# Performance work log

Measured on AMD Instinct MI355X. Metric: run time of the kernel, lower is better.

## Reference

```python
import jax, jax.numpy as jnp
import numpy as np
import math

B, S, DIM, H = 2, 2048, 1024, 16
DH = DIM // H          # 64, per-head dim
DFF = 2048             # FCLayer hidden
NEG = -1.0e9


def setup_inputs() -> dict:
    key = jax.random.key(0)
    ks = jax.random.split(key, 10)
    glorot = jax.nn.initializers.glorot_uniform()
    de_x = jax.random.normal(ks[0], (B, S, DIM), dtype=jnp.float32)
    en_x = jax.random.normal(ks[1], (B, S, DIM), dtype=jnp.float32)
    # causal mask: 1.0 where attention is disallowed (upper triangle)
    mask = jnp.triu(jnp.ones((S, S), dtype=jnp.float32), k=1)
    # Stacked per-head projection weights for the (shared) attn_heads.
    Wq = glorot(ks[2], (H, DIM, DH), jnp.float32)
    Wk = glorot(ks[3], (H, DIM, DH), jnp.float32)
    Wv = glorot(ks[4], (H, DIM, DH), jnp.float32)
    W1 = glorot(ks[5], (DIM, DFF), jnp.float32)
    b1 = jnp.zeros((DFF,), jnp.float32)
    W2 = glorot(ks[6], (DFF, DIM), jnp.float32)
    b2 = jnp.zeros((DIM,), jnp.float32)
    return {"de_x": de_x, "en_x": en_x, "mask": mask,
            "Wq": Wq, "Wk": Wk, "Wv": Wv,
            "W1": W1, "b1": b1, "W2": W2, "b2": b2}


def _multihead(q_x, k_x, v_x, Wq, Wk, Wv, mask):
    # q_x/k_x/v_x: [B,S,DIM]; W*: [H,DIM,DH]
    q = jnp.einsum('bsd,hde->bhse', q_x, Wq)
    k = jnp.einsum('bsd,hde->bhse', k_x, Wk)
    v = jnp.einsum('bsd,hde->bhse', v_x, Wv)
    p = jnp.einsum('bhse,bhte->bhst', q, k) / math.sqrt(DH)
    if mask is not None:
        p = p + mask * NEG
    p = jax.nn.softmax(p, axis=-1)
    h = jnp.einsum('bhst,bhte->bhse', p, v)      # [B,H,S,DH]
    # concat heads along feature dim -> [B,S,DIM]
    return h.transpose(0, 2, 1, 3).reshape(q_x.shape[0], q_x.shape[1], -1)


def reference(de_x, en_x, mask, Wq, Wk, Wv, W1, b1, W2, b2):
    # Faithful to the source: compute_multihead_output ignores its attn_heads
    # arg and always uses self.attn_heads, and binds head(q=outer_en, k=outer_en,
    # v=outer_de). So:
    #   h1 = MHA(q=de_x, k=de_x, v=de_x, mask) with attn_heads weights
    #   h2 = MHA(q=en_x, k=en_x, v=h1, None)   with the SAME weights
    h1 = _multihead(de_x, de_x, de_x, Wq, Wk, Wv, mask)
    h2 = _multihead(en_x, en_x, h1, Wq, Wk, Wv, None)
    ff1 = jax.nn.relu(h2 @ W1 + b1)
    y = ff1 @ W2 + b2
    return y
```

## Files before the change

### kernel.cpp

```cpp
#include <hip/hip_runtime.h>
#include <stdint.h>


#define DEV static __device__ __forceinline__

typedef __attribute__((ext_vector_type(8))) __bf16 bf16x8;
typedef __attribute__((ext_vector_type(8))) unsigned short u16x8;
typedef __attribute__((ext_vector_type(2))) uint32_t u32x2;
typedef __attribute__((ext_vector_type(4))) float f32x4;

DEV float bf2f(uint16_t u) { union { uint32_t u; float f; } v; v.u = ((uint32_t)u) << 16; return v.f; }
DEV uint16_t f2bf(float f) {
  union { float f; uint32_t u; } v; v.f = f;
  uint32_t r = v.u + 0x7fffu + ((v.u >> 16) & 1u);
  return (uint16_t)(r >> 16);
}
DEV uint16_t f2bf_hw(float f) { return __builtin_bit_cast(unsigned short, (__bf16)f); }

DEV bf16x8 asbf(u16x8 v) { return __builtin_bit_cast(bf16x8, v); }
DEV f32x4 mfma32(bf16x8 a, bf16x8 b, f32x4 c) {
  return __builtin_amdgcn_mfma_f32_16x16x32_bf16(a, b, c, 0, 0, 0);
}

DEV void gload_lds16(const void* g, void* l) {
  __builtin_amdgcn_global_load_lds(
      (const __attribute__((address_space(1))) uint32_t*)g,
      (__attribute__((address_space(3))) uint32_t*)l, 16, 0, 0);
}

DEV int swz(int row, int slot) { return slot ^ (row & 7); }

DEV bf16x8 frag8(const uint16_t* l, int row, int slot) {
  u16x8 v = *(const u16x8*)((const char*)l + row * 128 + (swz(row, slot) << 4));
  return asbf(v);
}

__global__ void probe_k(const uint32_t* __restrict__ mask, uint32_t* __restrict__ flag) {
  flag[0] = (mask[1] & 0xFFFFu) ? 1u : 0u;
}

__global__ __launch_bounds__(256) void cvt_k(const void* __restrict__ src,
                                             uint16_t* __restrict__ dst, int n,
                                             const uint32_t* __restrict__ flag) {
  const int isbf = (int)flag[0];
  const int stride = gridDim.x * 256 * 8;
  for (int i = (blockIdx.x * 256 + threadIdx.x) * 8; i < n; i += stride) {
    if (isbf) {
      *(u16x8*)(dst + i) = *(const u16x8*)((const uint16_t*)src + i);
    } else {
      const float* sf = (const float*)src + i;
      u16x8 o;
      for (int j = 0; j < 8; j++) o[j] = f2bf(sf[j]);
      *(u16x8*)(dst + i) = o;
    }
  }
}

__global__ __launch_bounds__(256) void transpose_k(const void* __restrict__ in_,
                                                   uint16_t* __restrict__ out, int R, int C,
                                                   float scale,
                                                   const uint32_t* __restrict__ flag) {
  __shared__ uint16_t t[32][33];
  const int isbf = (int)flag[0];
  const int b = blockIdx.z;
  const float* in_f = (const float*)in_ + (size_t)b * R * C;
  const uint16_t* in_u = (const uint16_t*)in_ + (size_t)b * R * C;
  out += (size_t)b * R * C;
  const int c0 = blockIdx.x * 32, r0 = blockIdx.y * 32;
  const int tx = threadIdx.x & 31, ty = threadIdx.x >> 5;
  for (int i = 0; i < 4; i++) {
    int r = ty + i * 8;
    size_t idx = (size_t)(r0 + r) * C + c0 + tx;
    uint16_t v;
    if (isbf) v = (scale == 1.0f) ? in_u[idx] : f2bf(bf2f(in_u[idx]) * scale);
    else      v = f2bf(in_f[idx] * scale);
    t[r][tx] = v;
  }
  __syncthreads();
  for (int i = 0; i < 4; i++) {
    int r = ty + i * 8;
    out[(size_t)(c0 + r) * R + r0 + tx] = t[tx][r];
  }
}

__global__ __launch_bounds__(256) void proj_k(
    const uint16_t* __restrict__ A_qk, const uint16_t* __restrict__ A_v,
    const uint16_t* __restrict__ Wt,
    uint16_t* __restrict__ Q, uint16_t* __restrict__ K, uint16_t* __restrict__ Vt) {
  __shared__ __attribute__((aligned(16))) uint16_t lA[2][128 * 64];
  __shared__ __attribute__((aligned(16))) uint16_t lB[2][128 * 64];
  const int tid = threadIdx.x, lane = tid & 63, wave = tid >> 6;
  const int g = lane >> 4;
  const int m0 = blockIdx.x * 128, n0 = blockIdx.y * 128;
  const int proj = n0 >> 10;
  const uint16_t* A = (proj == 2 ? A_v : A_qk);
  const uint16_t* Bt = Wt + (size_t)n0 * 1024;
  const int wm = wave >> 1, wn = wave & 1;
  f32x4 acc[4][4] = {};
  const int lrow = lane >> 3, sl = lane & 7;
  auto STAGE = [&](int buf, int kt) {
    for (int i = 0; i < 4; i++) {
      int cb = (i * 4 + wave) * 64;
      int row = (cb >> 3) + lrow;
      int so = swz(row, sl) << 3;
      gload_lds16(A + (size_t)(m0 + row) * 1024 + kt + so, &lA[buf][cb * 8]);
      gload_lds16(Bt + (size_t)row * 1024 + kt + so, &lB[buf][cb * 8]);
    }
  };
  STAGE(0, 0);
  int cur = 0;
  for (int it = 0; it < 16; it++) {
    __syncthreads();
    if (it + 1 < 16) STAGE(cur ^ 1, (it + 1) * 64);
    for (int kk = 0; kk < 2; kk++) {
      bf16x8 af[4], bfr[4];
      for (int fm = 0; fm < 4; fm++) af[fm] = frag8(lA[cur], wm * 64 + fm * 16 + (lane & 15), kk * 4 + g);
      for (int fn = 0; fn < 4; fn++) bfr[fn] = frag8(lB[cur], wn * 64 + fn * 16 + (lane & 15), kk * 4 + g);
      for (int fm = 0; fm < 4; fm++)
        for (int fn = 0; fn < 4; fn++)
          acc[fm][fn] = mfma32(af[fm], bfr[fn], acc[fm][fn]);
    }
    cur ^= 1;
  }
  if (proj != 2) {
    uint16_t* outp = (proj == 0 ? Q : K);
    for (int fm = 0; fm < 4; fm++)
      for (int fn = 0; fn < 4; fn++)
        for (int r = 0; r < 4; r++) {
          int row = m0 + wm * 64 + fm * 16 + g * 4 + r;
          int b = row >> 11, s = row & 2047;
          int col = n0 + wn * 64 + fn * 16 + (lane & 15);
          int h = (col >> 6) & 15, e = col & 63;
          outp[(((size_t)(b * 16 + h)) * 2048 + s) * 64 + e] = f2bf(acc[fm][fn][r]);
        }
  } else {
    __syncthreads();
    uint16_t* tv = &lA[0][0];
    for (int fm = 0; fm < 4; fm++)
      for (int fn = 0; fn < 4; fn++)
        for (int r = 0; r < 4; r++) {
          int rl = wm * 64 + fm * 16 + g * 4 + r;
          int cl = wn * 64 + fn * 16 + (lane & 15);
          int byte = rl * 2;
          *(uint16_t*)((char*)tv + cl * 256 + ((((byte >> 4)) ^ (cl & 15)) << 4) + (byte & 15)) =
              f2bf(acc[fm][fn][r]);
        }
    __syncthreads();
    const int b = m0 >> 11, s0 = m0 & 2047;
    const int c = tid >> 1, half = tid & 1;
    const int col = n0 + c;
    const int h = (col >> 6) & 15, e = col & 63;
    uint16_t* dst = Vt + (((size_t)(b * 16 + h)) * 64 + e) * 2048 + s0 + half * 64;
    for (int j = 0; j < 8; j++) {
      int rl = half * 64 + j * 8;
      u16x8 v = *(const u16x8*)((const char*)tv + c * 256 + (((rl >> 3) ^ (c & 15)) << 4));
      *(u16x8*)(dst + j * 8) = v;
    }
  }
}

template <int CAUSAL>
__global__ __launch_bounds__(256) void attn_k(const uint16_t* __restrict__ Q,
                                              const uint16_t* __restrict__ K,
                                              const uint16_t* __restrict__ Vt,
                                              uint16_t* __restrict__ Op0,
                                              uint16_t* __restrict__ Op1,
                                              float* __restrict__ lbuf) {
  __shared__ __attribute__((aligned(16))) uint16_t lK[2][64 * 64];
  __shared__ __attribute__((aligned(16))) uint16_t lV[2][64 * 64];
  __shared__ __attribute__((aligned(16))) uint16_t lP[4][16 * 64];
  const int tid = threadIdx.x, lane = tid & 63, wave = tid >> 6;
  const int g = lane >> 4;
  const int bx = blockIdx.x, h = blockIdx.y, b = blockIdx.z;
  int qt, split, kt0, kt1;
  if (CAUSAL) {
    if (bx < 32) {
      qt = 31 - (bx >> 1);
      split = bx & 1;
      int n0 = (qt + 1) >> 1;
      kt0 = split ? n0 : 0;
      kt1 = split ? (qt + 1) : n0;
    } else {
      qt = 47 - bx; split = 0; kt0 = 0; kt1 = qt + 1;
    }
  } else {
    qt = bx & 31; split = bx >> 5; kt0 = split * 16; kt1 = kt0 + 16;
  }
  const size_t bh = (size_t)(b * 16 + h);
  const uint16_t* Qg = Q + bh * 2048 * 64;
  const uint16_t* Kg = K + bh * 2048 * 64;
  const uint16_t* Vg = Vt + bh * 64 * 2048;
  uint16_t* lPw = lP[wave];
  bf16x8 ones;
  for (int j = 0; j < 8; j++) ones[j] = (__bf16)1.0f;
  const int lrow = lane >> 3, sl = lane & 7;
  auto STAGE = [&](int buf, int kt) {
    for (int i = 0; i < 2; i++) {
      int cb = (i * 4 + wave) * 64;
      int row = (cb >> 3) + lrow;
      int so = swz(row, sl) << 3;
      gload_lds16(Kg + (size_t)(kt * 64 + row) * 64 + so, &lK[buf][cb * 8]);
      gload_lds16(Vg + (size_t)row * 2048 + kt * 64 + so, &lV[buf][cb * 8]);
    }
  };
  const int q0 = qt * 64;
  bf16x8 qf[2];
  {
    int row = q0 + wave * 16 + (lane & 15);
    for (int kk = 0; kk < 2; kk++)
      qf[kk] = asbf(*(const u16x8*)(Qg + (size_t)row * 64 + kk * 32 + g * 8));
  }
  f32x4 oacc[4] = {};
  f32x4 acc_l = {};
  const int qrow = lane & 15;
  STAGE(0, kt0);
  int buf = 0;
  for (int kt = kt0; kt < kt1; kt++) {
    __syncthreads();
    if (kt + 1 < kt1) STAGE(buf ^ 1, kt + 1);
    f32x4 s[4] = {};
    for (int kk = 0; kk < 2; kk++)
      for (int nf = 0; nf < 4; nf++)
        s[nf] = mfma32(frag8(lK[buf], nf * 16 + (lane & 15), kk * 4 + g), qf[kk], s[nf]);
    if (CAUSAL && kt == qt) {
      for (int nf = 0; nf < 4; nf++)
        for (int r = 0; r < 4; r++) {
          int kloc = nf * 16 + g * 4 + r;
          if (kloc > wave * 16 + qrow) s[nf][r] = -1e9f;
        }
    }
    for (int nf = 0; nf < 4; nf++) {
      float p0 = __builtin_amdgcn_exp2f(s[nf][0]);
      float p1 = __builtin_amdgcn_exp2f(s[nf][1]);
      float p2 = __builtin_amdgcn_exp2f(s[nf][2]);
      float p3 = __builtin_amdgcn_exp2f(s[nf][3]);
      u32x2 w;
      w[0] = ((uint32_t)f2bf_hw(p1) << 16) | f2bf_hw(p0);
      w[1] = ((uint32_t)f2bf_hw(p3) << 16) | f2bf_hw(p2);
      int slot = 2 * nf + (g >> 1);
      *(u32x2*)((char*)lPw + qrow * 128 + ((slot ^ (qrow & 7)) << 4) + ((g & 1) << 3)) = w;
    }
    for (int kk = 0; kk < 2; kk++) {
      bf16x8 pa = frag8(lPw, qrow, kk * 4 + g);
      acc_l = mfma32(pa, ones, acc_l);
      for (int df = 0; df < 4; df++)
        oacc[df] = mfma32(pa, frag8(lV[buf], df * 16 + (lane & 15), kk * 4 + g), oacc[df]);
    }
    buf ^= 1;
  }
  uint16_t* Op = split ? Op1 : Op0;
  for (int df = 0; df < 4; df++)
    for (int r = 0; r < 4; r++) {
      int srow = q0 + wave * 16 + g * 4 + r;
      int e = df * 16 + (lane & 15);
      Op[((size_t)b * 2048 + srow) * 1024 + h * 64 + e] = f2bf(oacc[df][r]);
    }
  if ((lane & 15) == 0) {
    for (int r = 0; r < 4; r++) {
      int srow = q0 + wave * 16 + g * 4 + r;
      lbuf[((size_t)(split * 2 + b) * 16 + h) * 2048 + srow] = acc_l[r];
    }
  }
}

template <int CAUSAL>
__global__ __launch_bounds__(256) void merge_k(const uint16_t* __restrict__ O0,
                                               const uint16_t* __restrict__ O1,
                                               const float* __restrict__ lbuf,
                                               uint16_t* __restrict__ out) {
  int i = (blockIdx.x * 256 + threadIdx.x) * 8;
  int sg = i >> 10;
  int b = sg >> 11, s = sg & 2047;
  int h = (i & 1023) >> 6;
  size_t i0 = ((size_t)b * 16 + h) * 2048 + s;
  size_t i1 = ((size_t)(2 + b) * 16 + h) * 2048 + s;
  float l0 = lbuf[i0];
  u16x8 o0 = *(const u16x8*)(O0 + i);
  bool two = CAUSAL ? ((s >> 6) >= 16) : true;
  u16x8 o;
  if (two) {
    float inv = 1.f / (l0 + lbuf[i1]);
    u16x8 o1v = *(const u16x8*)(O1 + i);
    for (int j = 0; j < 8; j++)
      o[j] = f2bf((bf2f(o0[j]) + bf2f(o1v[j])) * inv);
  } else {
    float inv = 1.f / l0;
    for (int j = 0; j < 8; j++) o[j] = f2bf(bf2f(o0[j]) * inv);
  }
  *(u16x8*)(out + i) = o;
}

template <int RELU>
__global__ __launch_bounds__(256) void ff_k(const uint16_t* __restrict__ A,
                                            const uint16_t* __restrict__ Bt,
                                            const uint16_t* __restrict__ bias,
                                            uint16_t* __restrict__ C, int Kdim, int N) {
  __shared__ __attribute__((aligned(16))) uint16_t lA[2][128 * 64];
  __shared__ __attribute__((aligned(16))) uint16_t lB[2][128 * 64];
  const int tid = threadIdx.x, lane = tid & 63, wave = tid >> 6;
  const int g = lane >> 4;
  const int m0 = blockIdx.x * 128, n0 = blockIdx.y * 128;
  const int wm = wave >> 1, wn = wave & 1;
  f32x4 acc[4][4] = {};
  const int lrow = lane >> 3, sl = lane & 7;
  auto STAGE = [&](int buf, int kt) {
    for (int i = 0; i < 4; i++) {
      int cb = (i * 4 + wave) * 64;
      int row = (cb >> 3) + lrow;
      int so = swz(row, sl) << 3;
      gload_lds16(A + (size_t)(m0 + row) * Kdim + kt + so, &lA[buf][cb * 8]);
      gload_lds16(Bt + (size_t)(n0 + row) * Kdim + kt + so, &lB[buf][cb * 8]);
    }
  };
  STAGE(0, 0);
  int cur = 0;
  const int nit = Kdim >> 6;
  for (int it = 0; it < nit; it++) {
    __syncthreads();
    if (it + 1 < nit) STAGE(cur ^ 1, (it + 1) * 64);
    for (int kk = 0; kk < 2; kk++) {
      bf16x8 af[4], bfr[4];
      for (int fm = 0; fm < 4; fm++) af[fm] = frag8(lA[cur], wm * 64 + fm * 16 + (lane & 15), kk * 4 + g);
      for (int fn = 0; fn < 4; fn++) bfr[fn] = frag8(lB[cur], wn * 64 + fn * 16 + (lane & 15), kk * 4 + g);
      for (int fm = 0; fm < 4; fm++)
        for (int fn = 0; fn < 4; fn++)
          acc[fm][fn] = mfma32(af[fm], bfr[fn], acc[fm][fn]);
    }
    cur ^= 1;
  }
  for (int fm = 0; fm < 4; fm++)
    for (int fn = 0; fn < 4; fn++) {
      int col = n0 + wn * 64 + fn * 16 + (lane & 15);
      float bv = bf2f(bias[col]);
      for (int r = 0; r < 4; r++) {
        int row = m0 + wm * 64 + fm * 16 + g * 4 + r;
        float v = acc[fm][fn][r] + bv;
        if (RELU) v = fmaxf(v, 0.f);
        C[(size_t)row * N + col] = f2bf(v);
      }
    }
}

__global__ __launch_bounds__(256) void store_k(const uint16_t* __restrict__ yb,
                                               void* __restrict__ out, int n,
                                               const uint32_t* __restrict__ flag) {
  const int isbf = (int)flag[0];
  const int stride = gridDim.x * 256 * 8;
  for (int i = (blockIdx.x * 256 + threadIdx.x) * 8; i < n; i += stride) {
    u16x8 v = *(const u16x8*)(yb + i);
    if (isbf) {
      *(u16x8*)((uint16_t*)out + i) = v;
    } else {
      float* of = (float*)out + i;
      for (int j = 0; j < 8; j++) of[j] = bf2f(v[j]);
    }
  }
}

extern "C" void kernel_launch(void* const* d_in, const int* in_sizes, int n_in,
                              void* d_out, int out_size, void* d_ws, size_t ws_size,
                              hipStream_t stream) {
  const void* de_x = d_in[0];
  const void* en_x = d_in[1];
  const void* mask = d_in[2];
  const void* Wq = d_in[3];
  const void* Wk = d_in[4];
  const void* Wv = d_in[5];
  const void* W1 = d_in[6];
  const void* b1 = d_in[7];
  const void* W2 = d_in[8];
  const void* b2 = d_in[9];

  uint16_t* ws = (uint16_t*)d_ws;
  const size_t M1 = (size_t)1 << 20;
  uint32_t* flag = (uint32_t*)ws;
  uint16_t* b1c = ws + 1024;
  uint16_t* b2c = ws + 4096;
  float* lbuf = (float*)(ws + 8192);
  uint16_t* Wtq = ws + 1 * M1;
  uint16_t* Wtk = ws + 2 * M1;
  uint16_t* Wtv = ws + 3 * M1;
  uint16_t* W1t = ws + 4 * M1;
  uint16_t* W2t = ws + 6 * M1;
  uint16_t* de_c = ws + 8 * M1;
  uint16_t* en_c = ws + 12 * M1;
  uint16_t* Qb  = ws + 16 * M1;
  uint16_t* Kb  = ws + 20 * M1;
  uint16_t* Vtb = ws + 24 * M1;
  uint16_t* h1  = ws + 28 * M1;
  uint16_t* h2  = ws + 32 * M1;
  uint16_t* ff1 = Qb;
  uint16_t* yb  = Vtb;
  uint16_t* Op0 = de_c;
  uint16_t* Op1a = h2;
  uint16_t* Op1b = h1;

  const int NX = 2 * 2048 * 1024;
  dim3 blk(256);

  probe_k<<<1, 1, 0, stream>>>((const uint32_t*)mask, flag);
  cvt_k<<<2048, blk, 0, stream>>>(de_x, de_c, NX, flag);
  cvt_k<<<2048, blk, 0, stream>>>(en_x, en_c, NX, flag);
  cvt_k<<<1, blk, 0, stream>>>(b1, b1c, 2048, flag);
  cvt_k<<<1, blk, 0, stream>>>(b2, b2c, 1024, flag);
  transpose_k<<<dim3(2, 32, 16), blk, 0, stream>>>(Wq, Wtq, 1024, 64, 0.180336880f, flag);
  transpose_k<<<dim3(2, 32, 16), blk, 0, stream>>>(Wk, Wtk, 1024, 64, 1.0f, flag);
  transpose_k<<<dim3(2, 32, 16), blk, 0, stream>>>(Wv, Wtv, 1024, 64, 1.0f, flag);
  transpose_k<<<dim3(64, 32, 1), blk, 0, stream>>>(W1, W1t, 1024, 2048, 1.0f, flag);
  transpose_k<<<dim3(32, 64, 1), blk, 0, stream>>>(W2, W2t, 2048, 1024, 1.0f, flag);
  proj_k<<<dim3(32, 24), blk, 0, stream>>>(de_c, de_c, Wtq, Qb, Kb, Vtb);
  attn_k<1><<<dim3(48, 16, 2), blk, 0, stream>>>(Qb, Kb, Vtb, Op0, Op1a, lbuf);
  merge_k<1><<<2048, blk, 0, stream>>>(Op0, Op1a, lbuf, h1);
  proj_k<<<dim3(32, 24), blk, 0, stream>>>(en_c, h1, Wtq, Qb, Kb, Vtb);
  attn_k<0><<<dim3(64, 16, 2), blk, 0, stream>>>(Qb, Kb, Vtb, Op0, Op1b, lbuf);
  merge_k<0><<<2048, blk, 0, stream>>>(Op0, Op1b, lbuf, h2);
  ff_k<1><<<dim3(32, 16), blk, 0, stream>>>(h2, W1t, b1c, ff1, 1024, 2048);
  ff_k<0><<<dim3(32, 8), blk, 0, stream>>>(ff1, W2t, b2c, yb, 2048, 1024);
  store_k<<<2048, blk, 0, stream>>>(yb, d_out, out_size, flag);
}
```

Baseline: 294.3 us.

## Replace double-buffered LDS staging with single buffer in GEMM and attention kernels

Drops the LDS double buffering in the projection, attention and feed-forward kernels. Each iteration now loads its tile into one buffer, syncs, computes, then syncs again. This halves shared memory per block, which could allow more resident blocks per CU. In exchange, global-to-LDS loads no longer overlap with MFMA compute, and each iteration adds a second barrier.

```diff
diff --git a/kernel.cpp b/kernel.cpp
--- a/kernel.cpp
+++ b/kernel.cpp
@@ -87,8 +87,9 @@
     const uint16_t* __restrict__ A_qk, const uint16_t* __restrict__ A_v,
     const uint16_t* __restrict__ Wt,
     uint16_t* __restrict__ Q, uint16_t* __restrict__ K, uint16_t* __restrict__ Vt) {
-  __shared__ __attribute__((aligned(16))) uint16_t lA[2][128 * 64];
-  __shared__ __attribute__((aligned(16))) uint16_t lB[2][128 * 64];
+  __shared__ __attribute__((aligned(16))) uint16_t smem[2][128 * 64];
+  uint16_t* lA = smem[0];
+  uint16_t* lB = smem[1];
   const int tid = threadIdx.x, lane = tid & 63, wave = tid >> 6;
   const int g = lane >> 4;
   const int m0 = blockIdx.x * 128, n0 = blockIdx.y * 128;
@@ -98,29 +99,27 @@
   const int wm = wave >> 1, wn = wave & 1;
   f32x4 acc[4][4] = {};
   const int lrow = lane >> 3, sl = lane & 7;
-  auto STAGE = [&](int buf, int kt) {
+  auto STAGE = [&](int kt) {
     for (int i = 0; i < 4; i++) {
       int cb = (i * 4 + wave) * 64;
       int row = (cb >> 3) + lrow;
       int so = swz(row, sl) << 3;
-      gload_lds16(A + (size_t)(m0 + row) * 1024 + kt + so, &lA[buf][cb * 8]);
-      gload_lds16(Bt + (size_t)row * 1024 + kt + so, &lB[buf][cb * 8]);
+      gload_lds16(A + (size_t)(m0 + row) * 1024 + kt + so, &lA[cb * 8]);
+      gload_lds16(Bt + (size_t)row * 1024 + kt + so, &lB[cb * 8]);
     }
   };
-  STAGE(0, 0);
-  int cur = 0;
   for (int it = 0; it < 16; it++) {
-    __syncthreads();
-    if (it + 1 < 16) STAGE(cur ^ 1, (it + 1) * 64);
+    STAGE(it * 64);
+    __syncthreads();
     for (int kk = 0; kk < 2; kk++) {
       bf16x8 af[4], bfr[4];
-      for (int fm = 0; fm < 4; fm++) af[fm] = frag8(lA[cur], wm * 64 + fm * 16 + (lane & 15), kk * 4 + g);
-      for (int fn = 0; fn < 4; fn++) bfr[fn] = frag8(lB[cur], wn * 64 + fn * 16 + (lane & 15), kk * 4 + g);
+      for (int fm = 0; fm < 4; fm++) af[fm] = frag8(lA, wm * 64 + fm * 16 + (lane & 15), kk * 4 + g);
+      for (int fn = 0; fn < 4; fn++) bfr[fn] = frag8(lB, wn * 64 + fn * 16 + (lane & 15), kk * 4 + g);
       for (int fm = 0; fm < 4; fm++)
         for (int fn = 0; fn < 4; fn++)
           acc[fm][fn] = mfma32(af[fm], bfr[fn], acc[fm][fn]);
     }
-    cur ^= 1;
+    __syncthreads();
   }
   if (proj != 2) {
     uint16_t* outp = (proj == 0 ? Q : K);
@@ -134,8 +133,7 @@
           outp[(((size_t)(b * 16 + h)) * 2048 + s) * 64 + e] = f2bf(acc[fm][fn][r]);
         }
   } else {
-    __syncthreads();
-    uint16_t* tv = &lA[0][0];
+    uint16_t* tv = &smem[0][0];
     for (int fm = 0; fm < 4; fm++)
       for (int fn = 0; fn < 4; fn++)
         for (int r = 0; r < 4; r++) {
@@ -166,8 +164,8 @@
                                               uint16_t* __restrict__ Op0,
                                               uint16_t* __restrict__ Op1,
                                               float* __restrict__ lbuf) {
-  __shared__ __attribute__((aligned(16))) uint16_t lK[2][64 * 64];
-  __shared__ __attribute__((aligned(16))) uint16_t lV[2][64 * 64];
+  __shared__ __attribute__((aligned(16))) uint16_t lK[64 * 64];
+  __shared__ __attribute__((aligned(16))) uint16_t lV[64 * 64];
   __shared__ __attribute__((aligned(16))) uint16_t lP[4][16 * 64];
   const int tid = threadIdx.x, lane = tid & 63, wave = tid >> 6;
   const int g = lane >> 4;
@@ -194,13 +192,13 @@
   bf16x8 ones;
   for (int j = 0; j < 8; j++) ones[j] = (__bf16)1.0f;
   const int lrow = lane >> 3, sl = lane & 7;
-  auto STAGE = [&](int buf, int kt) {
+  auto STAGE = [&](int kt) {
     for (int i = 0; i < 2; i++) {
       int cb = (i * 4 + wave) * 64;
       int row = (cb >> 3) + lrow;
       int so = swz(row, sl) << 3;
-      gload_lds16(Kg + (size_t)(kt * 64 + row) * 64 + so, &lK[buf][cb * 8]);
-      gload_lds16(Vg + (size_t)row * 2048 + kt * 64 + so, &lV[buf][cb * 8]);
+      gload_lds16(Kg + (size_t)(kt * 64 + row) * 64 + so, &lK[cb * 8]);
+      gload_lds16(Vg + (size_t)row * 2048 + kt * 64 + so, &lV[cb * 8]);
     }
   };
   const int q0 = qt * 64;
@@ -213,15 +211,13 @@
   f32x4 oacc[4] = {};
   f32x4 acc_l = {};
   const int qrow = lane & 15;
-  STAGE(0, kt0);
-  int buf = 0;
   for (int kt = kt0; kt < kt1; kt++) {
-    __syncthreads();
-    if (kt + 1 < kt1) STAGE(buf ^ 1, kt + 1);
+    STAGE(kt);
+    __syncthreads();
     f32x4 s[4] = {};
     for (int kk = 0; kk < 2; kk++)
       for (int nf = 0; nf < 4; nf++)
-        s[nf] = mfma32(frag8(lK[buf], nf * 16 + (lane & 15), kk * 4 + g), qf[kk], s[nf]);
+        s[nf] = mfma32(frag8(lK, nf * 16 + (lane & 15), kk * 4 + g), qf[kk], s[nf]);
     if (CAUSAL && kt == qt) {
       for (int nf = 0; nf < 4; nf++)
         for (int r = 0; r < 4; r++) {
@@ -244,9 +240,9 @@
       bf16x8 pa = frag8(lPw, qrow, kk * 4 + g);
       acc_l = mfma32(pa, ones, acc_l);
       for (int df = 0; df < 4; df++)
-        oacc[df] = mfma32(pa, frag8(lV[buf], df * 16 + (lane & 15), kk * 4 + g), oacc[df]);
-    }
-    buf ^= 1;
+        oacc[df] = mfma32(pa, frag8(lV, df * 16 + (lane & 15), kk * 4 + g), oacc[df]);
+    }
+    __syncthreads();
   }
   uint16_t* Op = split ? Op1 : Op0;
   for (int df = 0; df < 4; df++)
@@ -295,38 +291,37 @@
                                             const uint16_t* __restrict__ Bt,
                                             const uint16_t* __restrict__ bias,
                                             uint16_t* __restrict__ C, int Kdim, int N) {
-  __shared__ __attribute__((aligned(16))) uint16_t lA[2][128 * 64];
-  __shared__ __attribute__((aligned(16))) uint16_t lB[2][128 * 64];
+  __shared__ __attribute__((aligned(16))) uint16_t smem[2][128 * 64];
+  uint16_t* lA = smem[0];
+  uint16_t* lB = smem[1];
   const int tid = threadIdx.x, lane = tid & 63, wave = tid >> 6;
   const int g = lane >> 4;
   const int m0 = blockIdx.x * 128, n0 = blockIdx.y * 128;
   const int wm = wave >> 1, wn = wave & 1;
   f32x4 acc[4][4] = {};
   const int lrow = lane >> 3, sl = lane & 7;
-  auto STAGE = [&](int buf, int kt) {
+  auto STAGE = [&](int kt) {
     for (int i = 0; i < 4; i++) {
       int cb = (i * 4 + wave) * 64;
       int row = (cb >> 3) + lrow;
       int so = swz(row, sl) << 3;
-      gload_lds16(A + (size_t)(m0 + row) * Kdim + kt + so, &lA[buf][cb * 8]);
-      gload_lds16(Bt + (size_t)(n0 + row) * Kdim + kt + so, &lB[buf][cb * 8]);
+      gload_lds16(A + (size_t)(m0 + row) * Kdim + kt + so, &lA[cb * 8]);
+      gload_lds16(Bt + (size_t)(n0 + row) * Kdim + kt + so, &lB[cb * 8]);
     }
   };
-  STAGE(0, 0);
-  int cur = 0;
   const int nit = Kdim >> 6;
   for (int it = 0; it < nit; it++) {
-    __syncthreads();
-    if (it + 1 < nit) STAGE(cur ^ 1, (it + 1) * 64);
+    STAGE(it * 64);
+    __syncthreads();
     for (int kk = 0; kk < 2; kk++) {
       bf16x8 af[4], bfr[4];
-      for (int fm = 0; fm < 4; fm++) af[fm] = frag8(lA[cur], wm * 64 + fm * 16 + (lane & 15), kk * 4 + g);
-      for (int fn = 0; fn < 4; fn++) bfr[fn] = frag8(lB[cur], wn * 64 + fn * 16 + (lane & 15), kk * 4 + g);
+      for (int fm = 0; fm < 4; fm++) af[fm] = frag8(lA, wm * 64 + fm * 16 + (lane & 15), kk * 4 + g);
+      for (int fn = 0; fn < 4; fn++) bfr[fn] = frag8(lB, wn * 64 + fn * 16 + (lane & 15), kk * 4 + g);
       for (int fm = 0; fm < 4; fm++)
         for (int fn = 0; fn < 4; fn++)
           acc[fm][fn] = mfma32(af[fm], bfr[fn], acc[fm][fn]);
     }
-    cur ^= 1;
+    __syncthreads();
   }
   for (int fm = 0; fm < 4; fm++)
     for (int fn = 0; fn < 4; fn++) {
```

Result: slower. 302.3 us (+2.7%).
